# Performance work log

Measured on AMD Instinct MI355X. Metric: run time of the kernel, lower is better.

Reference implementation:

```python
import jax, jax.numpy as jnp
import numpy as np

N = 8192
D_IN = 256
D_OUT = 256
E = 131072
P = 2  # number of bottom-to-up hierarchy levels


def gcn_conv(x, edge_index, W, b, num_nodes):
    """PyG-style GCNConv: add self-loops, symmetric normalization, x @ W + b."""
    loops = jnp.arange(num_nodes)
    src = jnp.concatenate([edge_index[0], loops])
    dst = jnp.concatenate([edge_index[1], loops])
    deg = jax.ops.segment_sum(jnp.ones_like(dst, dtype=x.dtype), dst,
                              num_segments=num_nodes)  # [N], >=1 due to self-loops
    dinv = jax.lax.rsqrt(deg)
    norm = dinv[src] * dinv[dst]                         # [E+N]
    h = x @ W                                            # [N, out]
    out = jax.ops.segment_sum(norm[:, None] * h[src], dst, num_segments=num_nodes)
    return out + b


def setup_inputs() -> dict:
    key = jax.random.key(0)
    ks = jax.random.split(key, 8)
    embedding = jax.random.normal(ks[0], (N, D_IN), dtype=jnp.float32)
    down2up_path = jax.random.uniform(ks[1], (P, N, N), dtype=jnp.float32)
    same_level_edge_index = jax.random.randint(ks[2], (2, E), 0, N)
    up2down_edge_index = jax.random.randint(ks[3], (2, E), 0, N)
    W_same = jax.random.normal(ks[4], (D_IN, D_OUT), dtype=jnp.float32) * (1.0 / np.sqrt(D_IN))
    b_same = jnp.zeros((D_OUT,), dtype=jnp.float32)
    W_top = jax.random.normal(ks[5], (D_OUT, D_OUT), dtype=jnp.float32) * (1.0 / np.sqrt(D_OUT))
    b_top = jnp.zeros((D_OUT,), dtype=jnp.float32)
    return {"embedding": embedding, "down2up_path": down2up_path,
            "same_level_edge_index": same_level_edge_index,
            "up2down_edge_index": up2down_edge_index,
            "W_same": W_same, "b_same": b_same,
            "W_top": W_top, "b_top": b_top}


def reference(embedding, down2up_path, same_level_edge_index, up2down_edge_index,
              W_same, b_same, W_top, b_top):
    # ---- bottom_to_up (MEAN path): per-level mm + residual add + row-mean normalize
    emb = embedding
    for p in range(down2up_path.shape[0]):  # small fixed number of hierarchy levels
        A = down2up_path[p]                  # [N, N]
        emb = (emb + A @ emb) * (1.0 / (A.sum(-1) + 1.0))[:, None]
    # ---- same-level GCNConv
    emb = gcn_conv(emb, same_level_edge_index, W_same, b_same, N)
    # ---- top_to_bottom GCNConv
    emb = gcn_conv(emb, up2down_edge_index, W_top, b_top, N)
    return emb
```

## Files before the change

### kernel.cpp

```cpp
#include <hip/hip_runtime.h>
#include <cstdint>

#define NN 8192
#define DD 256
#define KS 4

typedef unsigned short u16;
typedef __bf16 bf16x8 __attribute__((ext_vector_type(8)));
typedef float f32x4 __attribute__((ext_vector_type(4)));

__device__ __forceinline__ u16 f2bf(float f) {
    union { float f; unsigned u; } c; c.f = f;
    unsigned u = c.u;
    return (u16)((u + 0x7FFFu + ((u >> 16) & 1u)) >> 16);
}

__device__ __forceinline__ void cvt_store8(f32x4 a, f32x4 b, u16* dst) {
    union { u16 u[8]; uint4 v; } pk;
    pk.u[0] = f2bf(a[0]); pk.u[1] = f2bf(a[1]);
    pk.u[2] = f2bf(a[2]); pk.u[3] = f2bf(a[3]);
    pk.u[4] = f2bf(b[0]); pk.u[5] = f2bf(b[1]);
    pk.u[6] = f2bf(b[2]); pk.u[7] = f2bf(b[3]);
    *(uint4*)dst = pk.v;
}

template<bool AF32, bool ROWSUM>
__global__ __launch_bounds__(256, 2)
void gemm_k(const void* __restrict__ Ap, long ldA,
            const u16* __restrict__ BT, long ldBT,
            float* __restrict__ C, float* __restrict__ rs, int kPer)
{
    __shared__ __align__(16) u16 As[2][64 * 32];
    __shared__ __align__(16) u16 Bs[2][256 * 32];

    const int tid  = threadIdx.x;
    const int lane = tid & 63;
    const int wave = tid >> 6;
    const int r    = lane & 15;
    const int q    = lane >> 4;
    const long m0  = (long)blockIdx.x * 64;
    const long k0  = (long)blockIdx.z * kPer;
    float* __restrict__ Cs = C + (long)blockIdx.z * ((long)NN * DD);

    f32x4 acc[4][4] = {};
    f32x4 racc[4]   = {};
    bf16x8 ones;
    if constexpr (ROWSUM) {
        union { bf16x8 v; u16 u[8]; } cv;
        u16 pat = (r == 0) ? (u16)0x3F80 : (u16)0;
        #pragma unroll
        for (int j = 0; j < 8; ++j) cv.u[j] = pat;
        ones = cv.v;
    }

    const u16* bBase = BT + (long)(wave * 64 + r) * ldBT + k0 + q * 8;
    const int arow = tid >> 2;
    const int kq8  = tid & 3;
    const float* aBaseF = AF32 ? ((const float*)Ap + (m0 + arow) * ldA + k0 + kq8 * 8) : nullptr;
    u16* const aDst0 = &As[0][(arow >> 4) * 512 + (kq8 * 16 + (arow & 15)) * 8];
    u16* const aDst1 = &As[1][(arow >> 4) * 512 + (kq8 * 16 + (arow & 15)) * 8];
    const u16* aBaseH = AF32 ? nullptr
                             : ((const u16*)Ap + (m0 + wave * 16 + r) * ldA + k0 + q * 8);
    const int nsteps = kPer >> 5;

#define STAGE_B(t, buf) do {                                                      \
    const long koff_ = (long)(t) << 5;                                            \
    _Pragma("unroll")                                                             \
    for (int g2_ = 0; g2_ < 4; ++g2_)                                             \
        __builtin_amdgcn_global_load_lds(                                         \
            (const __attribute__((address_space(1))) void*)(bBase + (long)g2_ * 16 * ldBT + koff_), \
            (__attribute__((address_space(3))) void*)(&Bs[buf][(wave * 4 + g2_) * 512 + lane * 8]), \
            16, 0, 0);                                                            \
  } while (0)

#define STAGE_AH(t, buf)                                                          \
    __builtin_amdgcn_global_load_lds(                                             \
        (const __attribute__((address_space(1))) void*)(aBaseH + ((long)(t) << 5)), \
        (__attribute__((address_space(3))) void*)(&As[buf][wave * 512 + lane * 8]), \
        16, 0, 0)

    STAGE_B(0, 0);
    if constexpr (AF32) {
        f32x4 p0 = __builtin_nontemporal_load((const f32x4*)aBaseF);
        f32x4 p1 = __builtin_nontemporal_load((const f32x4*)(aBaseF + 4));
        cvt_store8(p0, p1, aDst0);
    } else {
        STAGE_AH(0, 0);
    }
    __syncthreads();

    for (int t = 0; t < nsteps; ++t) {
        const int cur = t & 1, nxt = cur ^ 1;
        const bool more = (t + 1 < nsteps);
        f32x4 na0, na1;
        if (more) {
            STAGE_B(t + 1, nxt);
            if constexpr (AF32) {
                const float* ap = aBaseF + ((long)(t + 1) << 5);
                na0 = __builtin_nontemporal_load((const f32x4*)ap);
                na1 = __builtin_nontemporal_load((const f32x4*)(ap + 4));
            } else {
                STAGE_AH(t + 1, nxt);
            }
        }
        bf16x8 af[4], bfr[4];
        #pragma unroll
        for (int i = 0; i < 4; ++i) {
            af[i]  = *(const bf16x8*)(&As[cur][i * 512 + lane * 8]);
            bfr[i] = *(const bf16x8*)(&Bs[cur][(wave * 4 + i) * 512 + lane * 8]);
        }
        #pragma unroll
        for (int i = 0; i < 4; ++i)
            #pragma unroll
            for (int j = 0; j < 4; ++j)
                acc[i][j] = __builtin_amdgcn_mfma_f32_16x16x32_bf16(af[i], bfr[j], acc[i][j], 0, 0, 0);
        if constexpr (ROWSUM) {
            if (wave == 0) {
                #pragma unroll
                for (int i = 0; i < 4; ++i)
                    racc[i] = __builtin_amdgcn_mfma_f32_16x16x32_bf16(af[i], ones, racc[i], 0, 0, 0);
            }
        }
        if constexpr (AF32) {
            if (more) cvt_store8(na0, na1, (nxt ? aDst1 : aDst0));
        }
        __syncthreads();
    }
#undef STAGE_B
#undef STAGE_AH

    #pragma unroll
    for (int i = 0; i < 4; ++i) {
        const long rowb = m0 + i * 16 + q * 4;
        #pragma unroll
        for (int j = 0; j < 4; ++j) {
            const long col = wave * 64 + j * 16 + r;
            #pragma unroll
            for (int rr2 = 0; rr2 < 4; ++rr2)
                Cs[(rowb + rr2) * DD + col] = acc[i][j][rr2];
        }
        if constexpr (ROWSUM) {
            if (wave == 0 && r == 0) {
                #pragma unroll
                for (int rr2 = 0; rr2 < 4; ++rr2)
                    rs[(long)blockIdx.z * NN + rowb + rr2] = racc[i][rr2];
            }
        }
    }
}

__global__ __launch_bounds__(256)
void tc_k(const float* __restrict__ src, u16* __restrict__ dst, int R, int C)
{
    __shared__ u16 t[64][72];
    const int tid = threadIdx.x;
    const int rr = tid >> 2;
    const int cc = (tid & 3) << 4;
    const long r0 = (long)blockIdx.x * 64;
    const long c0 = (long)blockIdx.y * 64;
    const float* sp = src + (r0 + rr) * C + c0 + cc;
    #pragma unroll
    for (int j = 0; j < 16; ++j) t[cc + j][rr] = f2bf(sp[j]);
    __syncthreads();
    u16* dp = dst + (c0 + rr) * (long)R + r0 + cc;
    #pragma unroll
    for (int j = 0; j < 16; ++j) dp[j] = t[rr][cc + j];
}

__global__ __launch_bounds__(256)
void tcw_k(const float* __restrict__ w0, const float* __restrict__ w1,
           u16* __restrict__ dst)
{
    __shared__ u16 t[64][72];
    const float* src = blockIdx.z ? w1 : w0;
    u16* d = dst + (size_t)blockIdx.z * DD * DD;
    const int tid = threadIdx.x;
    const int rr = tid >> 2;
    const int cc = (tid & 3) << 4;
    const long r0 = (long)blockIdx.x * 64;
    const long c0 = (long)blockIdx.y * 64;
    const float* sp = src + (r0 + rr) * DD + c0 + cc;
    #pragma unroll
    for (int j = 0; j < 16; ++j) t[cc + j][rr] = f2bf(sp[j]);
    __syncthreads();
    u16* dp = d + (c0 + rr) * (long)DD + r0 + cc;
    #pragma unroll
    for (int j = 0; j < 16; ++j) dp[j] = t[rr][cc + j];
}

__global__ __launch_bounds__(256)
void norm0_k(const float* __restrict__ Cacc, const float* __restrict__ rs,
             const float* __restrict__ resid,
             float* __restrict__ outF, u16* __restrict__ outT)
{
    __shared__ u16 t[64][72];
    const int tid = threadIdx.x;
    const int rr = tid >> 2;
    const int cc = (tid & 3) << 4;
    const long i0 = (long)blockIdx.x * 64;
    const int  n0 = blockIdx.y * 64;
    const long i  = i0 + rr;
    const float rsum = rs[i] + rs[NN + i] + rs[2 * NN + i] + rs[3 * NN + i];
    const float scale = 1.0f / (rsum + 1.0f);
    const float* c0p = Cacc + i * DD + n0 + cc;
    const float* rp  = resid + i * DD + n0 + cc;
    float* fp = outF + i * DD + n0 + cc;
    const long slab = (long)NN * DD;
    #pragma unroll
    for (int j = 0; j < 16; ++j) {
        float v = rp[j] + c0p[j] + c0p[j + slab] + c0p[j + 2 * slab] + c0p[j + 3 * slab];
        v *= scale;
        fp[j] = v;
        t[cc + j][rr] = f2bf(v);
    }
    __syncthreads();
    u16* op = outT + (long)(n0 + rr) * NN + i0 + cc;
    #pragma unroll
    for (int j = 0; j < 16; ++j) op[j] = t[rr][cc + j];
}

__global__ __launch_bounds__(256)
void norm1_k(const float* __restrict__ Cacc, const float* __restrict__ rs,
             const float* __restrict__ resid, u16* __restrict__ outR)
{
    const long g = ((long)blockIdx.x * 256 + threadIdx.x) * 4;
    const long row = g >> 8;
    const float rsum = rs[row] + rs[NN + row] + rs[2 * NN + row] + rs[3 * NN + row];
    const float scale = 1.0f / (rsum + 1.0f);
    const long slab = (long)NN * DD;
    const float4 c0 = *(const float4*)(Cacc + g);
    const float4 c1 = *(const float4*)(Cacc + g + slab);
    const float4 c2 = *(const float4*)(Cacc + g + 2 * slab);
    const float4 c3 = *(const float4*)(Cacc + g + 3 * slab);
    const float4 rv = *(const float4*)(resid + g);
    u16* op = outR + g;
    op[0] = f2bf((rv.x + c0.x + c1.x + c2.x + c3.x) * scale);
    op[1] = f2bf((rv.y + c0.y + c1.y + c2.y + c3.y) * scale);
    op[2] = f2bf((rv.z + c0.z + c1.z + c2.z + c3.z) * scale);
    op[3] = f2bf((rv.w + c0.w + c1.w + c2.w + c3.w) * scale);
}

__global__ __launch_bounds__(256)
void count2_k(const int* __restrict__ dS, const int* __restrict__ dU, int E,
              int* __restrict__ counts) {
    const int e = blockIdx.x * 256 + threadIdx.x;
    const int* d = blockIdx.y ? dU : dS;
    if (e < E) atomicAdd(counts + blockIdx.y * NN + d[e], 1);
}

__global__ __launch_bounds__(1024)
void scan2_k(const int* __restrict__ counts, int* __restrict__ offs,
             int* __restrict__ cursor, float* __restrict__ dinv) {
    const int p = blockIdx.x;
    const int* cnt = counts + p * NN;
    int* off   = offs + p * (NN + 1);
    int* curp  = cursor + p * NN;
    float* dv  = dinv + p * NN;

    __shared__ int wpre[17];
    __shared__ int sbase;
    const int tid  = threadIdx.x;
    const int lane = tid & 63;
    const int wid  = tid >> 6;
    if (tid == 0) { sbase = 0; wpre[0] = 0; }
    __syncthreads();
    for (int base = 0; base < NN; base += 1024) {
        const int c = cnt[base + tid];
        dv[base + tid] = 1.0f / sqrtf((float)c + 1.0f);
        int x = c;
        #pragma unroll
        for (int d = 1; d < 64; d <<= 1) {
            int y = __shfl_up(x, d, 64);
            if (lane >= d) x += y;
        }
        if (lane == 63) wpre[wid + 1] = x;
        __syncthreads();
        if (wid == 0) {
            int w = (lane < 16) ? wpre[lane + 1] : 0;
            #pragma unroll
            for (int d = 1; d < 16; d <<= 1) {
                int y = __shfl_up(w, d, 64);
                if (lane >= d) w += y;
            }
            if (lane < 16) wpre[lane + 1] = w;
        }
        __syncthreads();
        const int tot  = wpre[16];
        const int excl = sbase + wpre[wid] + (x - c);
        off[base + tid]  = excl;
        curp[base + tid] = excl;
        __syncthreads();
        if (tid == 0) sbase += tot;
    }
    if (tid == 0) off[NN] = sbase;
}

__global__ __launch_bounds__(256)
void fill2_k(const int* __restrict__ eiS, const int* __restrict__ eiU, int E,
             int* __restrict__ cursor, int* __restrict__ csr) {
    const int e = blockIdx.x * 256 + threadIdx.x;
    const int p = blockIdx.y;
    const int* src = p ? eiU : eiS;
    const int* dst = src + E;
    if (e < E) {
        int pos = atomicAdd(cursor + p * NN + dst[e], 1);
        csr[p * ((1 << 17) + NN) + pos] = src[e];
    }
}

__global__ __launch_bounds__(256)
void gather_k(const float* __restrict__ h,
              const int* __restrict__ offs,
              const int* __restrict__ csr,
              const float* __restrict__ dinv,
              const float* __restrict__ bias,
              u16* __restrict__ outBF,
              float* __restrict__ outF)
{
    const int node = blockIdx.x * 4 + (threadIdx.x >> 6);
    const int lane = threadIdx.x & 63;
    const float di = dinv[node];
    const float4 hs = ((const float4*)(h + (long)node * DD))[lane];
    const float s0 = di * di;
    float4 acc;
    acc.x = hs.x * s0; acc.y = hs.y * s0; acc.z = hs.z * s0; acc.w = hs.w * s0;

    const int b0 = offs[node], b1 = offs[node + 1];
    for (int base = b0; base < b1; base += 64) {
        const int nb = (b1 - base < 64) ? (b1 - base) : 64;
        int   sidx = node;
        float wv   = 0.0f;
        if (lane < nb) {
            sidx = csr[base + lane];
            wv   = di * dinv[sidx];
        }
        int e = 0;
        for (; e + 4 <= nb; e += 4) {
            const int   i0 = __shfl(sidx, e),     i1 = __shfl(sidx, e + 1);
            const int   i2 = __shfl(sidx, e + 2), i3 = __shfl(sidx, e + 3);
            const float w0 = __shfl(wv, e),       w1 = __shfl(wv, e + 1);
            const float w2 = __shfl(wv, e + 2),   w3 = __shfl(wv, e + 3);
            const float4 x0 = ((const float4*)(h + (long)i0 * DD))[lane];
            const float4 x1 = ((const float4*)(h + (long)i1 * DD))[lane];
            const float4 x2 = ((const float4*)(h + (long)i2 * DD))[lane];
            const float4 x3 = ((const float4*)(h + (long)i3 * DD))[lane];
            acc.x += w0 * x0.x + w1 * x1.x + w2 * x2.x + w3 * x3.x;
            acc.y += w0 * x0.y + w1 * x1.y + w2 * x2.y + w3 * x3.y;
            acc.z += w0 * x0.z + w1 * x1.z + w2 * x2.z + w3 * x3.z;
            acc.w += w0 * x0.w + w1 * x1.w + w2 * x2.w + w3 * x3.w;
        }
        for (; e < nb; ++e) {
            const int   s = __shfl(sidx, e);
            const float w = __shfl(wv, e);
            const float4 x = ((const float4*)(h + (long)s * DD))[lane];
            acc.x += w * x.x; acc.y += w * x.y; acc.z += w * x.z; acc.w += w * x.w;
        }
    }
    const float4 bv = ((const float4*)bias)[lane];
    acc.x += bv.x; acc.y += bv.y; acc.z += bv.z; acc.w += bv.w;

    if (outF) {
        ((float4*)(outF + (long)node * DD))[lane] = acc;
    } else {
        u16* op = outBF + (long)node * DD + lane * 4;
        op[0] = f2bf(acc.x); op[1] = f2bf(acc.y);
        op[2] = f2bf(acc.z); op[3] = f2bf(acc.w);
    }
}

extern "C" void kernel_launch(void* const* d_in, const int* in_sizes, int n_in,
                              void* d_out, int out_size, void* d_ws, size_t ws_size,
                              hipStream_t stream)
{
    (void)n_in; (void)out_size; (void)ws_size;
    const float* emb0  = (const float*)d_in[0];
    const float* A     = (const float*)d_in[1];
    const int*   eiS   = (const int*)d_in[2];
    const int*   eiU   = (const int*)d_in[3];
    const float* Wsame = (const float*)d_in[4];
    const float* bsame = (const float*)d_in[5];
    const float* Wtop  = (const float*)d_in[6];
    const float* btop  = (const float*)d_in[7];
    const int E = in_sizes[2] / 2;
    const int CSRSZ = (1 << 17) + NN;

    char* ws = (char*)d_ws;
    u16*   embT   = (u16*)  (ws + 0);
    float* Cacc   = (float*)(ws + 4194304);
    float* emb1   = (float*)(ws + 37748736);
    u16*   xbf    = (u16*)  (ws + 46137344);
    u16*   WT     = (u16*)  (ws + 50331648);
    float* rsb    = (float*)(ws + 50593792);
    float* dinv2  = (float*)(ws + 50724864);
    int*   counts = (int*)  (ws + 50790400);
    int*   offs2  = (int*)  (ws + 50855936);
    int*   cursor = (int*)  (ws + 50921488);
    int*   csr2   = (int*)  (ws + 50987024);

    const dim3 blk(256);
    const dim3 gDense(128, 1, KS), gGcn(128, 1, 1);
    const dim3 gE2((E + 255) / 256, 2), gG(NN / 4);

    tc_k<<<dim3(128, 4), blk, 0, stream>>>(emb0, embT, NN, DD);
    tcw_k<<<dim3(4, 4, 2), blk, 0, stream>>>(Wsame, Wtop, WT);
    hipMemsetAsync(counts, 0, 65536, stream);
    count2_k<<<gE2, blk, 0, stream>>>(eiS + E, eiU + E, E, counts);
    scan2_k<<<dim3(2), dim3(1024), 0, stream>>>(counts, offs2, cursor, dinv2);
    fill2_k<<<gE2, blk, 0, stream>>>(eiS, eiU, E, cursor, csr2);

    gemm_k<true, true><<<gDense, blk, 0, stream>>>(A, NN, embT, NN, Cacc, rsb, NN / KS);
    norm0_k<<<dim3(128, 4), blk, 0, stream>>>(Cacc, rsb, emb0, emb1, embT);

    gemm_k<true, true><<<gDense, blk, 0, stream>>>(A + (size_t)NN * NN, NN, embT, NN, Cacc, rsb, NN / KS);
    norm1_k<<<dim3(2048), blk, 0, stream>>>(Cacc, rsb, emb1, xbf);

    gemm_k<false, false><<<gGcn, blk, 0, stream>>>(xbf, DD, WT, DD, Cacc, nullptr, 256);
    gather_k<<<gG, blk, 0, stream>>>(Cacc, offs2, csr2, dinv2, bsame, xbf, nullptr);

    gemm_k<false, false><<<gGcn, blk, 0, stream>>>(xbf, DD, WT + DD * DD, DD, Cacc, nullptr, 256);
    gather_k<<<gG, blk, 0, stream>>>(Cacc, offs2 + (NN + 1), csr2 + CSRSZ,
                                     dinv2 + NN, btop, nullptr, (float*)d_out);
}
```

Baseline: 925.5 us.

## Raise split-K to 8, fuse transposes, and build CSR in one cooperative kernel

Doubles the split-K factor for the dense N×N GEMMs from 4 to 8, so the grid has 1024 blocks instead of 512, and the normalisation kernels now sum KS partial slabs. The two transpose kernels are merged into one launch. The memset plus the count, scan and fill kernels for CSR construction are replaced by one cooperative kernel that uses grid syncs and a two-level block scan. The bf16 conversion switches to the native cast. The extra split-K slabs double the fp32 partial buffer and the traffic in the reduction kernels, and the cooperative launch needs all 1024 blocks to be resident at once.

```diff
diff --git a/kernel.cpp b/kernel.cpp
--- a/kernel.cpp
+++ b/kernel.cpp
@@ -1,26 +1,29 @@
 #include <hip/hip_runtime.h>
+#include <hip/hip_cooperative_groups.h>
 #include <cstdint>
+
+namespace cg = cooperative_groups;
 
 #define NN 8192
 #define DD 256
-#define KS 4
+#define KS 8
+#define CSRSZ ((1 << 17) + NN)
 
 typedef unsigned short u16;
+typedef __bf16 bf16_t;
 typedef __bf16 bf16x8 __attribute__((ext_vector_type(8)));
 typedef float f32x4 __attribute__((ext_vector_type(4)));
 
 __device__ __forceinline__ u16 f2bf(float f) {
-    union { float f; unsigned u; } c; c.f = f;
-    unsigned u = c.u;
-    return (u16)((u + 0x7FFFu + ((u >> 16) & 1u)) >> 16);
+    union { bf16_t h; u16 u; } c; c.h = (bf16_t)f; return c.u;
 }
 
 __device__ __forceinline__ void cvt_store8(f32x4 a, f32x4 b, u16* dst) {
-    union { u16 u[8]; uint4 v; } pk;
-    pk.u[0] = f2bf(a[0]); pk.u[1] = f2bf(a[1]);
-    pk.u[2] = f2bf(a[2]); pk.u[3] = f2bf(a[3]);
-    pk.u[4] = f2bf(b[0]); pk.u[5] = f2bf(b[1]);
-    pk.u[6] = f2bf(b[2]); pk.u[7] = f2bf(b[3]);
+    union { bf16_t h[8]; uint4 v; } pk;
+    pk.h[0] = (bf16_t)a[0]; pk.h[1] = (bf16_t)a[1];
+    pk.h[2] = (bf16_t)a[2]; pk.h[3] = (bf16_t)a[3];
+    pk.h[4] = (bf16_t)b[0]; pk.h[5] = (bf16_t)b[1];
+    pk.h[6] = (bf16_t)b[2]; pk.h[7] = (bf16_t)b[3];
     *(uint4*)dst = pk.v;
 }
 
@@ -150,40 +153,31 @@
 }
 
 __global__ __launch_bounds__(256)
-void tc_k(const float* __restrict__ src, u16* __restrict__ dst, int R, int C)
+void trans_k(const float* __restrict__ emb0,
+             const float* __restrict__ w0, const float* __restrict__ w1,
+             u16* __restrict__ embT, u16* __restrict__ WT)
 {
     __shared__ u16 t[64][72];
+    const int b = blockIdx.x;
+    const float* src; u16* dst; long R, C, r0, c0;
+    if (b < 512) {
+        src = emb0; dst = embT; R = NN; C = DD;
+        r0 = (long)(b & 127) * 64; c0 = (long)(b >> 7) * 64;
+    } else {
+        const int w = b - 512;
+        const int which = w >> 4, tt = w & 15;
+        src = which ? w1 : w0; dst = WT + (size_t)which * DD * DD;
+        R = DD; C = DD;
+        r0 = (long)(tt & 3) * 64; c0 = (long)(tt >> 2) * 64;
+    }
     const int tid = threadIdx.x;
     const int rr = tid >> 2;
     const int cc = (tid & 3) << 4;
-    const long r0 = (long)blockIdx.x * 64;
-    const long c0 = (long)blockIdx.y * 64;
     const float* sp = src + (r0 + rr) * C + c0 + cc;
     #pragma unroll
     for (int j = 0; j < 16; ++j) t[cc + j][rr] = f2bf(sp[j]);
     __syncthreads();
-    u16* dp = dst + (c0 + rr) * (long)R + r0 + cc;
-    #pragma unroll
-    for (int j = 0; j < 16; ++j) dp[j] = t[rr][cc + j];
-}
-
-__global__ __launch_bounds__(256)
-void tcw_k(const float* __restrict__ w0, const float* __restrict__ w1,
-           u16* __restrict__ dst)
-{
-    __shared__ u16 t[64][72];
-    const float* src = blockIdx.z ? w1 : w0;
-    u16* d = dst + (size_t)blockIdx.z * DD * DD;
-    const int tid = threadIdx.x;
-    const int rr = tid >> 2;
-    const int cc = (tid & 3) << 4;
-    const long r0 = (long)blockIdx.x * 64;
-    const long c0 = (long)blockIdx.y * 64;
-    const float* sp = src + (r0 + rr) * DD + c0 + cc;
-    #pragma unroll
-    for (int j = 0; j < 16; ++j) t[cc + j][rr] = f2bf(sp[j]);
-    __syncthreads();
-    u16* dp = d + (c0 + rr) * (long)DD + r0 + cc;
+    u16* dp = dst + (c0 + rr) * R + r0 + cc;
     #pragma unroll
     for (int j = 0; j < 16; ++j) dp[j] = t[rr][cc + j];
 }
@@ -200,7 +194,9 @@
     const long i0 = (long)blockIdx.x * 64;
     const int  n0 = blockIdx.y * 64;
     const long i  = i0 + rr;
-    const float rsum = rs[i] + rs[NN + i] + rs[2 * NN + i] + rs[3 * NN + i];
+    float rsum = 0.0f;
+    #pragma unroll
+    for (int s2 = 0; s2 < KS; ++s2) rsum += rs[s2 * NN + i];
     const float scale = 1.0f / (rsum + 1.0f);
     const float* c0p = Cacc + i * DD + n0 + cc;
     const float* rp  = resid + i * DD + n0 + cc;
@@ -208,7 +204,9 @@
     const long slab = (long)NN * DD;
     #pragma unroll
     for (int j = 0; j < 16; ++j) {
-        float v = rp[j] + c0p[j] + c0p[j + slab] + c0p[j + 2 * slab] + c0p[j + 3 * slab];
+        float v = rp[j];
+        #pragma unroll
+        for (int s2 = 0; s2 < KS; ++s2) v += c0p[j + s2 * slab];
         v *= scale;
         fp[j] = v;
         t[cc + j][rr] = f2bf(v);
@@ -225,86 +223,102 @@
 {
     const long g = ((long)blockIdx.x * 256 + threadIdx.x) * 4;
     const long row = g >> 8;
-    const float rsum = rs[row] + rs[NN + row] + rs[2 * NN + row] + rs[3 * NN + row];
+    float rsum = 0.0f;
+    #pragma unroll
+    for (int s2 = 0; s2 < KS; ++s2) rsum += rs[s2 * NN + row];
     const float scale = 1.0f / (rsum + 1.0f);
     const long slab = (long)NN * DD;
-    const float4 c0 = *(const float4*)(Cacc + g);
-    const float4 c1 = *(const float4*)(Cacc + g + slab);
-    const float4 c2 = *(const float4*)(Cacc + g + 2 * slab);
-    const float4 c3 = *(const float4*)(Cacc + g + 3 * slab);
     const float4 rv = *(const float4*)(resid + g);
+    float vx = rv.x, vy = rv.y, vz = rv.z, vw = rv.w;
+    #pragma unroll
+    for (int s2 = 0; s2 < KS; ++s2) {
+        const float4 c = *(const float4*)(Cacc + g + s2 * slab);
+        vx += c.x; vy += c.y; vz += c.z; vw += c.w;
+    }
     u16* op = outR + g;
-    op[0] = f2bf((rv.x + c0.x + c1.x + c2.x + c3.x) * scale);
-    op[1] = f2bf((rv.y + c0.y + c1.y + c2.y + c3.y) * scale);
-    op[2] = f2bf((rv.z + c0.z + c1.z + c2.z + c3.z) * scale);
-    op[3] = f2bf((rv.w + c0.w + c1.w + c2.w + c3.w) * scale);
+    op[0] = f2bf(vx * scale);
+    op[1] = f2bf(vy * scale);
+    op[2] = f2bf(vz * scale);
+    op[3] = f2bf(vw * scale);
 }
 
 __global__ __launch_bounds__(256)
-void count2_k(const int* __restrict__ dS, const int* __restrict__ dU, int E,
-              int* __restrict__ counts) {
-    const int e = blockIdx.x * 256 + threadIdx.x;
-    const int* d = blockIdx.y ? dU : dS;
-    if (e < E) atomicAdd(counts + blockIdx.y * NN + d[e], 1);
-}
-
-__global__ __launch_bounds__(1024)
-void scan2_k(const int* __restrict__ counts, int* __restrict__ offs,
-             int* __restrict__ cursor, float* __restrict__ dinv) {
-    const int p = blockIdx.x;
-    const int* cnt = counts + p * NN;
-    int* off   = offs + p * (NN + 1);
-    int* curp  = cursor + p * NN;
-    float* dv  = dinv + p * NN;
-
-    __shared__ int wpre[17];
-    __shared__ int sbase;
-    const int tid  = threadIdx.x;
-    const int lane = tid & 63;
-    const int wid  = tid >> 6;
-    if (tid == 0) { sbase = 0; wpre[0] = 0; }
-    __syncthreads();
-    for (int base = 0; base < NN; base += 1024) {
-        const int c = cnt[base + tid];
-        dv[base + tid] = 1.0f / sqrtf((float)c + 1.0f);
+void csr_k(const int* __restrict__ eiS, const int* __restrict__ eiU, int E,
+           int* __restrict__ counts, int* __restrict__ offs,
+           int* __restrict__ cursor, float* __restrict__ dinv,
+           int* __restrict__ csr, int* __restrict__ csums)
+{
+    cg::grid_group grid = cg::this_grid();
+    const int tid = threadIdx.x;
+    const int gsz = gridDim.x * 256;
+    const int g   = blockIdx.x * 256 + tid;
+
+    for (int i = g; i < 2 * NN; i += gsz) counts[i] = 0;
+    grid.sync();
+
+    for (int i = g; i < 2 * E; i += gsz) {
+        const int p = (i >= E);
+        const int e = i - p * E;
+        const int* d = (p ? eiU : eiS) + E;
+        atomicAdd(counts + p * NN + d[e], 1);
+    }
+    grid.sync();
+
+    __shared__ int wsum[4];
+    if (blockIdx.x < (2 * NN) / 256) {
+        const int chunk = blockIdx.x;
+        const int p   = chunk >> 5;
+        const int idx = chunk * 256 + tid;
+        const int li  = idx - p * NN;
+        const int c = counts[idx];
+        dinv[idx] = 1.0f / sqrtf((float)c + 1.0f);
+        const int lane = tid & 63, wid = tid >> 6;
         int x = c;
         #pragma unroll
-        for (int d = 1; d < 64; d <<= 1) {
-            int y = __shfl_up(x, d, 64);
-            if (lane >= d) x += y;
-        }
-        if (lane == 63) wpre[wid + 1] = x;
+        for (int d2 = 1; d2 < 64; d2 <<= 1) {
+            int y = __shfl_up(x, d2, 64);
+            if (lane >= d2) x += y;
+        }
+        if (lane == 63) wsum[wid] = x;
         __syncthreads();
-        if (wid == 0) {
-            int w = (lane < 16) ? wpre[lane + 1] : 0;
-            #pragma unroll
-            for (int d = 1; d < 16; d <<= 1) {
-                int y = __shfl_up(w, d, 64);
-                if (lane >= d) w += y;
-            }
-            if (lane < 16) wpre[lane + 1] = w;
-        }
-        __syncthreads();
-        const int tot  = wpre[16];
-        const int excl = sbase + wpre[wid] + (x - c);
-        off[base + tid]  = excl;
-        curp[base + tid] = excl;
-        __syncthreads();
-        if (tid == 0) sbase += tot;
-    }
-    if (tid == 0) off[NN] = sbase;
-}
-
-__global__ __launch_bounds__(256)
-void fill2_k(const int* __restrict__ eiS, const int* __restrict__ eiU, int E,
-             int* __restrict__ cursor, int* __restrict__ csr) {
-    const int e = blockIdx.x * 256 + threadIdx.x;
-    const int p = blockIdx.y;
-    const int* src = p ? eiU : eiS;
-    const int* dst = src + E;
-    if (e < E) {
-        int pos = atomicAdd(cursor + p * NN + dst[e], 1);
-        csr[p * ((1 << 17) + NN) + pos] = src[e];
+        int base = 0;
+        #pragma unroll
+        for (int wv = 0; wv < 3; ++wv) if (wv < wid) base += wsum[wv];
+        offs[p * (NN + 1) + li] = base + x - c;
+        if (tid == 255) csums[chunk] = base + x;
+    }
+    grid.sync();
+
+    if (blockIdx.x == 0 && tid < 64) {
+        const int lane = tid;
+        const int v = csums[lane];
+        int x = v;
+        #pragma unroll
+        for (int d2 = 1; d2 < 32; d2 <<= 1) {
+            int y = __shfl_up(x, d2, 64);
+            if ((lane & 31) >= d2) x += y;
+        }
+        csums[lane] = x - v;
+        if (lane == 31) offs[NN] = x;
+        if (lane == 63) offs[(NN + 1) + NN] = x;
+    }
+    grid.sync();
+
+    for (int i = g; i < 2 * NN; i += gsz) {
+        const int p  = i >> 13;
+        const int li = i & (NN - 1);
+        const int v = offs[p * (NN + 1) + li] + csums[i >> 8];
+        offs[p * (NN + 1) + li] = v;
+        cursor[i] = v;
+    }
+    grid.sync();
+
+    for (int i = g; i < 2 * E; i += gsz) {
+        const int p = (i >= E);
+        const int e = i - p * E;
+        const int* srcl = p ? eiU : eiS;
+        const int pos = atomicAdd(cursor + p * NN + srcl[E + e], 1);
+        csr[p * CSRSZ + pos] = srcl[e];
     }
 }
 
@@ -382,31 +396,33 @@
     const float* Wtop  = (const float*)d_in[6];
     const float* btop  = (const float*)d_in[7];
     const int E = in_sizes[2] / 2;
-    const int CSRSZ = (1 << 17) + NN;
 
     char* ws = (char*)d_ws;
     u16*   embT   = (u16*)  (ws + 0);
     float* Cacc   = (float*)(ws + 4194304);
-    float* emb1   = (float*)(ws + 37748736);
-    u16*   xbf    = (u16*)  (ws + 46137344);
-    u16*   WT     = (u16*)  (ws + 50331648);
-    float* rsb    = (float*)(ws + 50593792);
-    float* dinv2  = (float*)(ws + 50724864);
-    int*   counts = (int*)  (ws + 50790400);
-    int*   offs2  = (int*)  (ws + 50855936);
-    int*   cursor = (int*)  (ws + 50921488);
-    int*   csr2   = (int*)  (ws + 50987024);
+    float* emb1   = (float*)(ws + 71303168);
+    u16*   xbf    = (u16*)  (ws + 79691776);
+    u16*   WT     = (u16*)  (ws + 83886080);
+    float* rsb    = (float*)(ws + 84148224);
+    float* dinv2  = (float*)(ws + 84410368);
+    int*   counts = (int*)  (ws + 84475904);
+    int*   offs2  = (int*)  (ws + 84541440);
+    int*   cursor = (int*)  (ws + 84607232);
+    int*   csums  = (int*)  (ws + 84672768);
+    int*   csr2   = (int*)  (ws + 84673280);
 
     const dim3 blk(256);
     const dim3 gDense(128, 1, KS), gGcn(128, 1, 1);
-    const dim3 gE2((E + 255) / 256, 2), gG(NN / 4);
-
-    tc_k<<<dim3(128, 4), blk, 0, stream>>>(emb0, embT, NN, DD);
-    tcw_k<<<dim3(4, 4, 2), blk, 0, stream>>>(Wsame, Wtop, WT);
-    hipMemsetAsync(counts, 0, 65536, stream);
-    count2_k<<<gE2, blk, 0, stream>>>(eiS + E, eiU + E, E, counts);
-    scan2_k<<<dim3(2), dim3(1024), 0, stream>>>(counts, offs2, cursor, dinv2);
-    fill2_k<<<gE2, blk, 0, stream>>>(eiS, eiU, E, cursor, csr2);
+    const dim3 gG(NN / 4);
+
+    trans_k<<<dim3(544), blk, 0, stream>>>(emb0, Wsame, Wtop, embT, WT);
+    {
+        const int* a0 = eiS; const int* a1 = eiU; int a2 = E;
+        int* a3 = counts; int* a4 = offs2; int* a5 = cursor;
+        float* a6 = dinv2; int* a7 = csr2; int* a8 = csums;
+        void* args[] = { &a0, &a1, &a2, &a3, &a4, &a5, &a6, &a7, &a8 };
+        hipLaunchCooperativeKernel((const void*)csr_k, dim3(1024), blk, args, 0, stream);
+    }
 
     gemm_k<true, true><<<gDense, blk, 0, stream>>>(A, NN, embT, NN, Cacc, rsb, NN / KS);
     norm0_k<<<dim3(128, 4), blk, 0, stream>>>(Cacc, rsb, emb0, emb1, embT);
```

New measurement: 1.474 ms. 59.3% more time.
